# Kernel tuning notes

Measured on AMD Instinct MI355X. Metric: run time of the kernel, lower is better.

The kernel has to match this reference:

```python
import jax, jax.numpy as jnp
import numpy as np

N = 50000        # nodes
E = 800000       # edges (before self-loops)
A_DIM = 128      # attribute dim (= a_hid)
S_DIM = 64       # structural dim (= s_hid)
L = 4            # num_layers


def setup_inputs() -> dict:
    key = jax.random.key(0)
    ks = jax.random.split(key, 10)
    sc = 0.05
    return {
        "x": jax.random.normal(ks[0], (N, A_DIM), jnp.float32),
        "s": jax.random.normal(ks[1], (N, S_DIM), jnp.float32),
        "edge_index": jax.random.randint(ks[2], (2, E), 0, N, dtype=jnp.int64),
        "gcn_W": jax.random.normal(ks[3], (L, A_DIM, A_DIM), jnp.float32) * sc,
        "gcn_b": jnp.zeros((L, A_DIM), jnp.float32),
        "gna_w1W": jax.random.normal(ks[4], (L, S_DIM, S_DIM), jnp.float32) * sc,
        "gna_w1b": jnp.zeros((L, S_DIM), jnp.float32),
        "gna_w2W": jax.random.normal(ks[5], (L, S_DIM, S_DIM), jnp.float32) * sc,
        "gna_w2b": jnp.zeros((L, S_DIM), jnp.float32),
        "gna_a": jax.random.normal(ks[6], (L, S_DIM), jnp.float32) * sc,
    }


def _gelu(v):
    return jax.nn.gelu(v, approximate=False)  # matches torch F.gelu default


def _self_loops(edge_index, n):
    loop = jnp.arange(n, dtype=edge_index.dtype)
    row = jnp.concatenate([edge_index[0], loop])  # src
    col = jnp.concatenate([edge_index[1], loop])  # dst
    return row, col


def _guide_forward(x, s, edge_index, gcn_W, gcn_b,
                   gna_w1W, gna_w1b, gna_w2W, gna_w2b, gna_a):
    n = x.shape[0]
    row, col = _self_loops(edge_index, n)  # [E+N]

    # ---- attribute autoencoder: GCN with symmetric normalization ----
    deg = jax.ops.segment_sum(jnp.ones_like(col, dtype=x.dtype), col, num_segments=n)
    dinv = jnp.where(deg > 0, jax.lax.rsqrt(deg), 0.0)
    norm = dinv[row] * dinv[col]                       # [E+N]
    h = x
    for i in range(L):
        h2 = h @ gcn_W[i]                              # [N, A]
        agg = jax.ops.segment_sum(norm[:, None] * h2[row], col, num_segments=n)
        h = agg + gcn_b[i]
        if i < L - 1:                                  # jk=None: no act after last
            h = _gelu(h)

    # ---- structure autoencoder: GNA with edge-softmax attention ----
    g = s
    for i in range(L):
        t = g @ gna_w2W[i] + gna_w2b[i]                # w2(s), [N, S]
        # alpha_e = (t_dst - t_src) @ a, softmax over edges grouped by dst
        alpha = (t[col] - t[row]) @ gna_a[i]           # [E+N]
        amax = jax.ops.segment_max(alpha, col, num_segments=n)
        e = jnp.exp(alpha - amax[col])
        denom = jax.ops.segment_sum(e, col, num_segments=n)
        w = e / (denom[col] + 1e-16)
        msg = jax.ops.segment_sum(w[:, None] * t[row], col, num_segments=n)
        out = g @ gna_w1W[i] + gna_w1b[i] + msg
        g = _gelu(out)                                 # act applied after every layer
    return h, g


def reference(x, s, edge_index, gcn_W, gcn_b,
              gna_w1W, gna_w1b, gna_w2W, gna_w2b, gna_a):
    return _guide_forward(x, s, edge_index, gcn_W, gcn_b,
                          gna_w1W, gna_w1b, gna_w2W, gna_w2b, gna_a)
```

## Files before the change

### kernel.cpp

```cpp
#include <hip/hip_runtime.h>
#include <hip/hip_fp16.h>
#include <math.h>

#define N_NODES 50000
#define E_EDGES 800000
#define ET (E_EDGES + N_NODES)
#define L_LAYERS 4
#define NB_SCAN ((N_NODES + 255) / 256)
#define MF2_BLOCKS ((N_NODES + 127) / 128)
#define AGG_BLOCKS ((N_NODES / 2 * 64 + 255) / 256)

typedef __attribute__((ext_vector_type(8))) short short8;
typedef __attribute__((ext_vector_type(4))) float f32x4;

__device__ __forceinline__ float gelu_f(float x) {
    float z = fabsf(x) * 0.70710678118654752f;
    float t = __fdividef(1.0f, fmaf(0.3275911f, z, 1.0f));
    float p = t * fmaf(t, fmaf(t, fmaf(t, fmaf(t, 1.061405429f, -1.453152027f),
                                       1.421413741f), -0.284496736f),
                       0.254829592f);
    float e = __expf(-z * z);
    float erfz = copysignf(fmaf(-p, e, 1.0f), x);
    return 0.5f * x * (1.0f + erfz);
}

__device__ __forceinline__ void split_hl(float x, unsigned short& h, unsigned short& lo) {
    unsigned u = __float_as_uint(x);
    h = (unsigned short)(u >> 16);
    float hif = __uint_as_float(u & 0xffff0000u);
    lo = (unsigned short)(__float_as_uint(x - hif) >> 16);
}

__device__ __forceinline__ void fma8h(const float4& raw, float m, float* acc) {
    const __half2* h = reinterpret_cast<const __half2*>(&raw);
#pragma unroll
    for (int i = 0; i < 4; ++i) {
        float2 f = __half22float2(h[i]);
        acc[2 * i]     = fmaf(f.x, m, acc[2 * i]);
        acc[2 * i + 1] = fmaf(f.y, m, acc[2 * i + 1]);
    }
}


__global__ __launch_bounds__(256) void count_pos(const int* __restrict__ ecol,
                                                 int* __restrict__ cnt,
                                                 int* __restrict__ aux) {
    int e = blockIdx.x * 256 + threadIdx.x;
    if (e >= ET) return;
    int c = (e < E_EDGES) ? ecol[e] : (e - E_EDGES);
    aux[e] = atomicAdd(&cnt[c], 1);
}

__global__ __launch_bounds__(256) void scan_part1(const int* __restrict__ cnt,
                                                  int* __restrict__ bsum) {
    __shared__ int red[256];
    int t = threadIdx.x;
    int i = blockIdx.x * 256 + t;
    red[t] = (i < N_NODES) ? cnt[i] : 0;
    __syncthreads();
#pragma unroll
    for (int off = 128; off; off >>= 1) {
        if (t < off) red[t] += red[t + off];
        __syncthreads();
    }
    if (t == 0) bsum[blockIdx.x] = red[0];
}

__global__ __launch_bounds__(256) void scan_part3(const int* __restrict__ cnt,
                                                  const int* __restrict__ bsum,
                                                  int* __restrict__ ptrb,
                                                  float* __restrict__ dinv) {
    __shared__ int red[256];
    __shared__ int sh[256];
    int t = threadIdx.x;
    red[t] = (t < (int)blockIdx.x) ? bsum[t] : 0;
    __syncthreads();
#pragma unroll
    for (int off = 128; off; off >>= 1) {
        if (t < off) red[t] += red[t + off];
        __syncthreads();
    }
    int base = red[0];
    int i = blockIdx.x * 256 + t;
    int v = (i < N_NODES) ? cnt[i] : 0;
    sh[t] = v;
    __syncthreads();
    for (int off = 1; off < 256; off <<= 1) {
        int u = (t >= off) ? sh[t - off] : 0;
        __syncthreads();
        sh[t] += u;
        __syncthreads();
    }
    int excl = sh[t] - v + base;
    if (i < N_NODES) {
        ptrb[i] = excl;
        dinv[i] = rsqrtf((float)v);
    }
    if (i == N_NODES - 1) ptrb[N_NODES] = excl + v;
}

__global__ __launch_bounds__(256) void bucket(const int* __restrict__ erow,
                                              const int* __restrict__ ecol,
                                              const int* __restrict__ aux,
                                              const int* __restrict__ ptrb,
                                              int* __restrict__ eidx) {
    int e = blockIdx.x * 256 + threadIdx.x;
    if (e >= ET) return;
    int r, c;
    if (e < E_EDGES) { r = erow[e]; c = ecol[e]; }
    else             { r = e - E_EDGES; c = r; }
    int pos = ptrb[c] + aux[e];
    eidx[pos] = r;
}


__global__ __launch_bounds__(256) void prep_w(const float* __restrict__ gcn_W,
                                              const float* __restrict__ w1W,
                                              const float* __restrict__ w2W,
                                              unsigned short* __restrict__ gf_hi,
                                              unsigned short* __restrict__ gf_lo,
                                              unsigned short* __restrict__ nf_hi,
                                              unsigned short* __restrict__ nf_lo) {
    int idx = blockIdx.x * 256 + threadIdx.x;
    if (idx < 8192) {
        int lane = idx & 63, nt = (idx >> 6) & 7, s = (idx >> 9) & 3, layer = idx >> 11;
        int q = lane >> 4, n = lane & 15;
        const float* W = gcn_W + (size_t)layer * 128 * 128;
        size_t o = (size_t)idx * 8;
#pragma unroll
        for (int j = 0; j < 8; ++j) {
            float x = W[(size_t)(s * 32 + q * 8 + j) * 128 + nt * 16 + n];
            unsigned short h, lo;
            split_hl(x, h, lo);
            gf_hi[o + j] = h; gf_lo[o + j] = lo;
        }
    } else if (idx < 8192 + 4096) {
        int t = idx - 8192;
        int lane = t & 63, nt = (t >> 6) & 7, s = (t >> 9) & 1, layer = t >> 10;
        int q = lane >> 4, n = lane & 15;
        int col = nt * 16 + n;
        const float* W = (col < 64) ? (w1W + (size_t)layer * 64 * 64)
                                    : (w2W + (size_t)layer * 64 * 64);
        int c = col & 63;
        size_t o = (size_t)t * 8;
#pragma unroll
        for (int j = 0; j < 8; ++j) {
            float x = W[(size_t)(s * 32 + q * 8 + j) * 64 + c];
            unsigned short h, lo;
            split_hl(x, h, lo);
            nf_hi[o + j] = h; nf_lo[o + j] = lo;
        }
    }
}


__device__ __forceinline__ void mfma_steps2(const float* __restrict__ A, int Kfull,
                                            int nsteps,
                                            const unsigned short* __restrict__ wfh,
                                            const unsigned short* __restrict__ wfl,
                                            const int* arow, const bool* avalid,
                                            int lq, int l, f32x4 acc[2][8]) {
    for (int s = 0; s < nsteps; ++s) {
        short8 ah[2], al[2];
#pragma unroll
        for (int g = 0; g < 2; ++g) {
            float4 a0 = make_float4(0.f, 0.f, 0.f, 0.f);
            float4 a1 = make_float4(0.f, 0.f, 0.f, 0.f);
            if (avalid[g]) {
                const float* ap = A + (size_t)arow[g] * Kfull + s * 32 + lq * 8;
                a0 = *(const float4*)ap;
                a1 = *(const float4*)(ap + 4);
            }
            float xs[8] = {a0.x, a0.y, a0.z, a0.w, a1.x, a1.y, a1.z, a1.w};
#pragma unroll
            for (int c = 0; c < 8; ++c) {
                unsigned short h, lo;
                split_hl(xs[c], h, lo);
                ah[g][c] = (short)h; al[g][c] = (short)lo;
            }
        }
#pragma unroll
        for (int nt = 0; nt < 8; ++nt) {
            size_t fo = ((size_t)(s * 8 + nt) * 64 + l) * 8;
            short8 wh = *(const short8*)(wfh + fo);
            short8 wl = *(const short8*)(wfl + fo);
#pragma unroll
            for (int g = 0; g < 2; ++g) {
                acc[g][nt] = __builtin_amdgcn_mfma_f32_16x16x32_bf16(ah[g], wh, acc[g][nt], 0, 0, 0);
                acc[g][nt] = __builtin_amdgcn_mfma_f32_16x16x32_bf16(ah[g], wl, acc[g][nt], 0, 0, 0);
                acc[g][nt] = __builtin_amdgcn_mfma_f32_16x16x32_bf16(al[g], wh, acc[g][nt], 0, 0, 0);
            }
        }
    }
}


__global__ __launch_bounds__(256) void gemm_both(
    const float* __restrict__ A0, const float* __restrict__ A1,
    const unsigned short* __restrict__ gfh, const unsigned short* __restrict__ gfl,
    const unsigned short* __restrict__ nfh, const unsigned short* __restrict__ nfl,
    const float* __restrict__ b1, const float* __restrict__ b2,
    const float* __restrict__ avec, const float* __restrict__ dinv,
    __half* __restrict__ h2, float* __restrict__ baseb,
    __half* __restrict__ ut, float* __restrict__ ub) {
    int tid = threadIdx.x;
    int w  = tid >> 6;
    int l  = tid & 63;
    int lq = l >> 4;
    int ln = l & 15;
    bool isg = blockIdx.x >= MF2_BLOCKS;
    int blk = isg ? (blockIdx.x - MF2_BLOCKS) : blockIdx.x;
    int m0 = blk * 128;
    int arow[2];
    bool avalid[2];
#pragma unroll
    for (int g = 0; g < 2; ++g) {
        arow[g] = m0 + w * 32 + g * 16 + ln;
        avalid[g] = arow[g] < N_NODES;
    }

    f32x4 acc[2][8];
#pragma unroll
    for (int g = 0; g < 2; ++g)
#pragma unroll
        for (int i = 0; i < 8; ++i) acc[g][i] = (f32x4){0.f, 0.f, 0.f, 0.f};

    if (!isg) {
        mfma_steps2(A0, 128, 4, gfh, gfl, arow, avalid, lq, l, acc);
#pragma unroll
        for (int g = 0; g < 2; ++g) {
            float dv[4];
#pragma unroll
            for (int r = 0; r < 4; ++r) {
                int row = m0 + w * 32 + g * 16 + lq * 4 + r;
                dv[r] = (row < N_NODES) ? dinv[row] : 0.f;
            }
#pragma unroll
            for (int nt = 0; nt < 8; ++nt) {
                int col = nt * 16 + ln;
#pragma unroll
                for (int r = 0; r < 4; ++r) {
                    int row = m0 + w * 32 + g * 16 + lq * 4 + r;
                    if (row < N_NODES)
                        h2[(size_t)row * 128 + col] = __float2half(acc[g][nt][r] * dv[r]);
                }
            }
        }
    } else {
        mfma_steps2(A1, 64, 2, nfh, nfl, arow, avalid, lq, l, acc);
#pragma unroll
        for (int g = 0; g < 2; ++g) {
#pragma unroll
            for (int nt = 0; nt < 4; ++nt) {
                int col = nt * 16 + ln;
                float bb = b1[col];
#pragma unroll
                for (int r = 0; r < 4; ++r) {
                    int row = m0 + w * 32 + g * 16 + lq * 4 + r;
                    if (row < N_NODES) baseb[(size_t)row * 64 + col] = acc[g][nt][r] + bb;
                }
            }
            float pa[4] = {0.f, 0.f, 0.f, 0.f};
            float t2s[4][4];
#pragma unroll
            for (int nt = 4; nt < 8; ++nt) {
                int col = (nt - 4) * 16 + ln;
                float bb = b2[col];
                float av = avec[col];
#pragma unroll
                for (int r = 0; r < 4; ++r) {
                    float t2 = acc[g][nt][r] + bb;
                    t2s[nt - 4][r] = t2;
                    pa[r] += t2 * av;
                }
            }
#pragma unroll
            for (int r = 0; r < 4; ++r) {
                pa[r] += __shfl_xor(pa[r], 1);
                pa[r] += __shfl_xor(pa[r], 2);
                pa[r] += __shfl_xor(pa[r], 4);
                pa[r] += __shfl_xor(pa[r], 8);
            }
            float ur[4];
#pragma unroll
            for (int r = 0; r < 4; ++r) ur[r] = expf(-pa[r]);
#pragma unroll
            for (int nt = 0; nt < 4; ++nt) {
                int col = nt * 16 + ln;
#pragma unroll
                for (int r = 0; r < 4; ++r) {
                    int row = m0 + w * 32 + g * 16 + lq * 4 + r;
                    if (row < N_NODES)
                        ut[(size_t)row * 64 + col] = __float2half(t2s[nt][r] * ur[r]);
                }
            }
            if (ln == 0) {
#pragma unroll
                for (int r = 0; r < 4; ++r) {
                    int row = m0 + w * 32 + g * 16 + lq * 4 + r;
                    if (row < N_NODES) ub[row] = ur[r];
                }
            }
        }
    }
}


__global__ __launch_bounds__(256) void agg_gcn(const __half* __restrict__ h2,
                                               const int* __restrict__ ptrb,
                                               const int* __restrict__ eidx,
                                               const float* __restrict__ dinv,
                                               const float* __restrict__ bias,
                                               float* __restrict__ out,
                                               int apply_gelu) {
    int widx = (blockIdx.x * 256 + (int)threadIdx.x) >> 6;
    int lane = threadIdx.x & 63;
    int half = lane >> 5;
    int hl   = lane & 31;
    int dst  = widx * 2 + half;
    if (dst >= N_NODES) return;
    int sub = hl >> 4;
    int fl  = hl & 15;
    int p0 = ptrb[dst], p1 = ptrb[dst + 1];
    float acc[8];
#pragma unroll
    for (int i = 0; i < 8; ++i) acc[i] = 0.f;
    for (int p = p0; p < p1; p += 32) {
        int nb = min(32, p1 - p);
        int srcs = (hl < nb) ? eidx[p + hl] : 0;
        for (int eb = 0; eb < nb; eb += 16) {
            int   sv[8];
            float mk[8];
#pragma unroll
            for (int k = 0; k < 8; ++k) {
                int e = eb + sub + 2 * k;
                int c = half * 32 + min(e, nb - 1);
                sv[k] = __shfl(srcs, c);
                mk[k] = (e < nb) ? 1.f : 0.f;
            }
            float4 raw[8];
#pragma unroll
            for (int k = 0; k < 8; ++k)
                raw[k] = *(const float4*)(h2 + (size_t)sv[k] * 128 + fl * 8);
#pragma unroll
            for (int k = 0; k < 8; ++k) fma8h(raw[k], mk[k], acc);
        }
    }
#pragma unroll
    for (int i = 0; i < 8; ++i) acc[i] += __shfl_xor(acc[i], 16);
    {
        float dd = dinv[dst];
        int c0 = fl * 8 + 4 * sub;
        float4 bb = *(const float4*)(bias + c0);
        float v0 = fmaf(dd, acc[4 * sub + 0], bb.x);
        float v1 = fmaf(dd, acc[4 * sub + 1], bb.y);
        float v2 = fmaf(dd, acc[4 * sub + 2], bb.z);
        float v3 = fmaf(dd, acc[4 * sub + 3], bb.w);
        if (apply_gelu) {
            v0 = gelu_f(v0); v1 = gelu_f(v1); v2 = gelu_f(v2); v3 = gelu_f(v3);
        }
        *(float4*)(out + (size_t)dst * 128 + c0) = make_float4(v0, v1, v2, v3);
    }
}


__global__ __launch_bounds__(256) void gna_agg(const __half* __restrict__ ut,
                                               const float* __restrict__ ub,
                                               const int* __restrict__ ptrb,
                                               const int* __restrict__ eidx,
                                               const float* __restrict__ base,
                                               float* __restrict__ gout) {
    int widx = (blockIdx.x * 256 + (int)threadIdx.x) >> 6;
    int lane = threadIdx.x & 63;
    int half = lane >> 5;
    int hl   = lane & 31;
    int dst  = widx * 2 + half;
    if (dst >= N_NODES) return;
    int sub = hl >> 3;
    int fl  = hl & 7;
    int p0 = ptrb[dst], p1 = ptrb[dst + 1];
    float se = 0.f;
    float acc[8];
#pragma unroll
    for (int i = 0; i < 8; ++i) acc[i] = 0.f;
    for (int p = p0; p < p1; p += 32) {
        int nb = min(32, p1 - p);
        int srcs = (hl < nb) ? eidx[p + hl] : 0;
        if (hl < nb) se += ub[srcs];
        int   sv[8];
        float mk[8];
#pragma unroll
        for (int k = 0; k < 8; ++k) {
            int e = sub + 4 * k;
            int c = half * 32 + min(e, nb - 1);
            sv[k] = __shfl(srcs, c);
            mk[k] = (e < nb) ? 1.f : 0.f;
        }
        float4 raw[8];
#pragma unroll
        for (int k = 0; k < 8; ++k)
            raw[k] = *(const float4*)(ut + (size_t)sv[k] * 64 + fl * 8);
#pragma unroll
        for (int k = 0; k < 8; ++k) fma8h(raw[k], mk[k], acc);
    }
#pragma unroll
    for (int off = 1; off <= 16; off <<= 1) se += __shfl_xor(se, off);
#pragma unroll
    for (int off = 8; off <= 16; off <<= 1)
#pragma unroll
        for (int i = 0; i < 8; ++i) acc[i] += __shfl_xor(acc[i], off);
    {
        float winv = __fdividef(1.0f, se + 1e-16f);
        int c0 = fl * 8 + 2 * sub;
        float2 bs = *(const float2*)(base + (size_t)dst * 64 + c0);
        float v0 = gelu_f(fmaf(acc[2 * sub + 0], winv, bs.x));
        float v1 = gelu_f(fmaf(acc[2 * sub + 1], winv, bs.y));
        *(float2*)(gout + (size_t)dst * 64 + c0) = make_float2(v0, v1);
    }
}


extern "C" void kernel_launch(void* const* d_in, const int* in_sizes, int n_in,
                              void* d_out, int out_size, void* d_ws, size_t ws_size,
                              hipStream_t stream) {
    const float* x     = (const float*)d_in[0];
    const float* s     = (const float*)d_in[1];
    const int*   ei    = (const int*)d_in[2];
    const float* gcn_W = (const float*)d_in[3];
    const float* gcn_b = (const float*)d_in[4];
    const float* w1W   = (const float*)d_in[5];
    const float* w1b   = (const float*)d_in[6];
    const float* w2W   = (const float*)d_in[7];
    const float* w2b   = (const float*)d_in[8];
    const float* ga    = (const float*)d_in[9];

    float* h_out = (float*)d_out;
    float* g_out = (float*)d_out + (size_t)N_NODES * 128;

    size_t off = 0;
    char* wsb = (char*)d_ws;
    auto take = [&](size_t bytes) {
        void* p = wsb + off;
        off = (off + bytes + 255) & ~(size_t)255;
        return p;
    };
    int*    cnt     = (int*)take((size_t)N_NODES * 4);
    int*    ptrb    = (int*)take((size_t)(N_NODES + 1) * 4);
    int*    aux     = (int*)take((size_t)ET * 4);
    float*  dinv    = (float*)take((size_t)N_NODES * 4);
    int*    eidx    = (int*)take((size_t)ET * 4);
    __half* h2      = (__half*)take((size_t)N_NODES * 128 * 2);
    __half* utbuf   = (__half*)take((size_t)N_NODES * 64 * 2);
    float*  basebuf = (float*)take((size_t)N_NODES * 64 * 4);
    float*  ubuf    = (float*)take((size_t)N_NODES * 4);
    int*    bsum    = (int*)take((size_t)NB_SCAN * 4);
    unsigned short* gf_hi = (unsigned short*)take((size_t)8192 * 8 * 2);
    unsigned short* gf_lo = (unsigned short*)take((size_t)8192 * 8 * 2);
    unsigned short* nf_hi = (unsigned short*)take((size_t)4096 * 8 * 2);
    unsigned short* nf_lo = (unsigned short*)take((size_t)4096 * 8 * 2);
    (void)ws_size; (void)in_sizes; (void)n_in; (void)out_size;

    const int* erow = ei;
    const int* ecol = ei + E_EDGES;

    hipMemsetAsync(cnt, 0, (size_t)N_NODES * 4, stream);

    int ge = (ET + 255) / 256;
    count_pos<<<ge, 256, 0, stream>>>(ecol, cnt, aux);
    scan_part1<<<NB_SCAN, 256, 0, stream>>>(cnt, bsum);
    scan_part3<<<NB_SCAN, 256, 0, stream>>>(cnt, bsum, ptrb, dinv);
    bucket<<<ge, 256, 0, stream>>>(erow, ecol, aux, ptrb, eidx);
    prep_w<<<48, 256, 0, stream>>>(gcn_W, w1W, w2W, gf_hi, gf_lo, nf_hi, nf_lo);

    const float* hin = x;
    const float* gin = s;
    for (int l = 0; l < L_LAYERS; ++l) {
        gemm_both<<<2 * MF2_BLOCKS, 256, 0, stream>>>(
            hin, gin,
            gf_hi + (size_t)l * 4 * 8 * 64 * 8, gf_lo + (size_t)l * 4 * 8 * 64 * 8,
            nf_hi + (size_t)l * 2 * 8 * 64 * 8, nf_lo + (size_t)l * 2 * 8 * 64 * 8,
            w1b + (size_t)l * 64, w2b + (size_t)l * 64, ga + (size_t)l * 64, dinv,
            h2, basebuf, utbuf, ubuf);
        agg_gcn<<<AGG_BLOCKS, 256, 0, stream>>>(
            h2, ptrb, eidx, dinv, gcn_b + (size_t)l * 128, h_out,
            (l < L_LAYERS - 1) ? 1 : 0);
        gna_agg<<<AGG_BLOCKS, 256, 0, stream>>>(
            utbuf, ubuf, ptrb, eidx, basebuf, g_out);
        hin = h_out;
        gin = g_out;
    }
}
```

Before: 480.1 us.

## Stage GEMM input and output tiles through LDS with 64-row blocks

The fused GEMM kernel now uses 64-row tiles instead of 128, which doubles the block count and halves the per-wave accumulator state. Input rows are loaded cooperatively into padded shared memory, and MFMA operands are read from there rather than gathered per lane from global memory. Results are written back through shared memory so global stores are full 16-byte row segments instead of scattered 2- or 4-byte stores. The cost is extra barriers and LDS traffic, and the weight fragments are now reread for every 64 rows rather than every 128.

```diff
diff --git a/kernel.cpp b/kernel.cpp
--- a/kernel.cpp
+++ b/kernel.cpp
@@ -7,7 +7,7 @@
 #define ET (E_EDGES + N_NODES)
 #define L_LAYERS 4
 #define NB_SCAN ((N_NODES + 255) / 256)
-#define MF2_BLOCKS ((N_NODES + 127) / 128)
+#define MF_BLOCKS ((N_NODES + 63) / 64)
 #define AGG_BLOCKS ((N_NODES / 2 * 64 + 255) / 256)
 
 typedef __attribute__((ext_vector_type(8))) short short8;
@@ -154,42 +154,32 @@
 }
 
 
-__device__ __forceinline__ void mfma_steps2(const float* __restrict__ A, int Kfull,
-                                            int nsteps,
-                                            const unsigned short* __restrict__ wfh,
-                                            const unsigned short* __restrict__ wfl,
-                                            const int* arow, const bool* avalid,
-                                            int lq, int l, f32x4 acc[2][8]) {
+__device__ __forceinline__ void mfma_steps_lds(const float* __restrict__ lda, int ldp,
+                                               int nsteps,
+                                               const unsigned short* __restrict__ wfh,
+                                               const unsigned short* __restrict__ wfl,
+                                               int lrow, int lq, int l,
+                                               f32x4* acc) {
     for (int s = 0; s < nsteps; ++s) {
-        short8 ah[2], al[2];
-#pragma unroll
-        for (int g = 0; g < 2; ++g) {
-            float4 a0 = make_float4(0.f, 0.f, 0.f, 0.f);
-            float4 a1 = make_float4(0.f, 0.f, 0.f, 0.f);
-            if (avalid[g]) {
-                const float* ap = A + (size_t)arow[g] * Kfull + s * 32 + lq * 8;
-                a0 = *(const float4*)ap;
-                a1 = *(const float4*)(ap + 4);
-            }
-            float xs[8] = {a0.x, a0.y, a0.z, a0.w, a1.x, a1.y, a1.z, a1.w};
-#pragma unroll
-            for (int c = 0; c < 8; ++c) {
-                unsigned short h, lo;
-                split_hl(xs[c], h, lo);
-                ah[g][c] = (short)h; al[g][c] = (short)lo;
-            }
+        const float* ap = lda + lrow * ldp + s * 32 + lq * 8;
+        float4 a0 = *(const float4*)ap;
+        float4 a1 = *(const float4*)(ap + 4);
+        float xs[8] = {a0.x, a0.y, a0.z, a0.w, a1.x, a1.y, a1.z, a1.w};
+        short8 ah, al;
+#pragma unroll
+        for (int c = 0; c < 8; ++c) {
+            unsigned short h, lo;
+            split_hl(xs[c], h, lo);
+            ah[c] = (short)h; al[c] = (short)lo;
         }
 #pragma unroll
         for (int nt = 0; nt < 8; ++nt) {
             size_t fo = ((size_t)(s * 8 + nt) * 64 + l) * 8;
             short8 wh = *(const short8*)(wfh + fo);
             short8 wl = *(const short8*)(wfl + fo);
-#pragma unroll
-            for (int g = 0; g < 2; ++g) {
-                acc[g][nt] = __builtin_amdgcn_mfma_f32_16x16x32_bf16(ah[g], wh, acc[g][nt], 0, 0, 0);
-                acc[g][nt] = __builtin_amdgcn_mfma_f32_16x16x32_bf16(ah[g], wl, acc[g][nt], 0, 0, 0);
-                acc[g][nt] = __builtin_amdgcn_mfma_f32_16x16x32_bf16(al[g], wh, acc[g][nt], 0, 0, 0);
-            }
+            acc[nt] = __builtin_amdgcn_mfma_f32_16x16x32_bf16(ah, wh, acc[nt], 0, 0, 0);
+            acc[nt] = __builtin_amdgcn_mfma_f32_16x16x32_bf16(ah, wl, acc[nt], 0, 0, 0);
+            acc[nt] = __builtin_amdgcn_mfma_f32_16x16x32_bf16(al, wh, acc[nt], 0, 0, 0);
         }
     }
 }
@@ -203,36 +193,50 @@
     const float* __restrict__ avec, const float* __restrict__ dinv,
     __half* __restrict__ h2, float* __restrict__ baseb,
     __half* __restrict__ ut, float* __restrict__ ub) {
+    __shared__ __align__(16) char smem[33792];
     int tid = threadIdx.x;
     int w  = tid >> 6;
     int l  = tid & 63;
     int lq = l >> 4;
     int ln = l & 15;
-    bool isg = blockIdx.x >= MF2_BLOCKS;
-    int blk = isg ? (blockIdx.x - MF2_BLOCKS) : blockIdx.x;
-    int m0 = blk * 128;
-    int arow[2];
-    bool avalid[2];
-#pragma unroll
-    for (int g = 0; g < 2; ++g) {
-        arow[g] = m0 + w * 32 + g * 16 + ln;
-        avalid[g] = arow[g] < N_NODES;
-    }
-
-    f32x4 acc[2][8];
-#pragma unroll
-    for (int g = 0; g < 2; ++g)
-#pragma unroll
-        for (int i = 0; i < 8; ++i) acc[g][i] = (f32x4){0.f, 0.f, 0.f, 0.f};
+    bool isg = blockIdx.x >= MF_BLOCKS;
+    int blk = isg ? (blockIdx.x - MF_BLOCKS) : blockIdx.x;
+    int m0 = blk * 64;
+    const float* A = isg ? A1 : A0;
+    const int Kfull = isg ? 64 : 128;
+    const int ldp   = isg ? 68 : 132;
+    float* lda = (float*)smem;
+
+    {
+        int row = tid >> 2, q = tid & 3;
+        int grow = m0 + row;
+        int hw = Kfull >> 2;
+        float4* dst = (float4*)(lda + row * ldp + q * hw);
+        int nv = hw >> 2;
+        if (grow < N_NODES) {
+            const float4* src = (const float4*)(A + (size_t)grow * Kfull + q * hw);
+            for (int i = 0; i < nv; ++i) dst[i] = src[i];
+        } else {
+            for (int i = 0; i < nv; ++i) dst[i] = make_float4(0.f, 0.f, 0.f, 0.f);
+        }
+    }
+    __syncthreads();
+
+    f32x4 acc[8];
+#pragma unroll
+    for (int i = 0; i < 8; ++i) acc[i] = (f32x4){0.f, 0.f, 0.f, 0.f};
+
+    int lrow = w * 16 + ln;
 
     if (!isg) {
-        mfma_steps2(A0, 128, 4, gfh, gfl, arow, avalid, lq, l, acc);
-#pragma unroll
-        for (int g = 0; g < 2; ++g) {
+        mfma_steps_lds(lda, 132, 4, gfh, gfl, lrow, lq, l, acc);
+        __syncthreads();
+        __half* ldc = (__half*)smem;
+        {
             float dv[4];
 #pragma unroll
             for (int r = 0; r < 4; ++r) {
-                int row = m0 + w * 32 + g * 16 + lq * 4 + r;
+                int row = m0 + w * 16 + lq * 4 + r;
                 dv[r] = (row < N_NODES) ? dinv[row] : 0.f;
             }
 #pragma unroll
@@ -240,24 +244,36 @@
                 int col = nt * 16 + ln;
 #pragma unroll
                 for (int r = 0; r < 4; ++r) {
-                    int row = m0 + w * 32 + g * 16 + lq * 4 + r;
-                    if (row < N_NODES)
-                        h2[(size_t)row * 128 + col] = __float2half(acc[g][nt][r] * dv[r]);
+                    int lr = w * 16 + lq * 4 + r;
+                    ldc[lr * 128 + col] = __float2half(acc[nt][r] * dv[r]);
                 }
             }
         }
+        __syncthreads();
+        {
+            int row = tid >> 2, seg = tid & 3;
+            int grow = m0 + row;
+            if (grow < N_NODES) {
+                const uint4* src = (const uint4*)(ldc + row * 128 + seg * 32);
+                uint4* dst = (uint4*)(h2 + (size_t)grow * 128 + seg * 32);
+#pragma unroll
+                for (int i = 0; i < 4; ++i) dst[i] = src[i];
+            }
+        }
     } else {
-        mfma_steps2(A1, 64, 2, nfh, nfl, arow, avalid, lq, l, acc);
-#pragma unroll
-        for (int g = 0; g < 2; ++g) {
+        mfma_steps_lds(lda, 68, 2, nfh, nfl, lrow, lq, l, acc);
+        __syncthreads();
+        float* ldf = (float*)smem;
+        __half* ldh = (__half*)(smem + 16384);
+        {
 #pragma unroll
             for (int nt = 0; nt < 4; ++nt) {
                 int col = nt * 16 + ln;
                 float bb = b1[col];
 #pragma unroll
                 for (int r = 0; r < 4; ++r) {
-                    int row = m0 + w * 32 + g * 16 + lq * 4 + r;
-                    if (row < N_NODES) baseb[(size_t)row * 64 + col] = acc[g][nt][r] + bb;
+                    int lr = w * 16 + lq * 4 + r;
+                    ldf[lr * 64 + col] = acc[nt][r] + bb;
                 }
             }
             float pa[4] = {0.f, 0.f, 0.f, 0.f};
@@ -269,7 +285,7 @@
                 float av = avec[col];
 #pragma unroll
                 for (int r = 0; r < 4; ++r) {
-                    float t2 = acc[g][nt][r] + bb;
+                    float t2 = acc[nt][r] + bb;
                     t2s[nt - 4][r] = t2;
                     pa[r] += t2 * av;
                 }
@@ -289,17 +305,31 @@
                 int col = nt * 16 + ln;
 #pragma unroll
                 for (int r = 0; r < 4; ++r) {
-                    int row = m0 + w * 32 + g * 16 + lq * 4 + r;
-                    if (row < N_NODES)
-                        ut[(size_t)row * 64 + col] = __float2half(t2s[nt][r] * ur[r]);
+                    int lr = w * 16 + lq * 4 + r;
+                    ldh[lr * 64 + col] = __float2half(t2s[nt][r] * ur[r]);
                 }
             }
             if (ln == 0) {
 #pragma unroll
                 for (int r = 0; r < 4; ++r) {
-                    int row = m0 + w * 32 + g * 16 + lq * 4 + r;
+                    int row = m0 + w * 16 + lq * 4 + r;
                     if (row < N_NODES) ub[row] = ur[r];
                 }
+            }
+        }
+        __syncthreads();
+        {
+            int row = tid >> 2, seg = tid & 3;
+            int grow = m0 + row;
+            if (grow < N_NODES) {
+                const uint4* src = (const uint4*)(ldf + row * 64 + seg * 16);
+                uint4* dst = (uint4*)(baseb + (size_t)grow * 64 + seg * 16);
+#pragma unroll
+                for (int i = 0; i < 4; ++i) dst[i] = src[i];
+                const uint4* srh = (const uint4*)(ldh + row * 64 + seg * 16);
+                uint4* dsh = (uint4*)(ut + (size_t)grow * 64 + seg * 16);
+#pragma unroll
+                for (int i = 0; i < 2; ++i) dsh[i] = srh[i];
             }
         }
     }
@@ -475,7 +505,7 @@
     const float* hin = x;
     const float* gin = s;
     for (int l = 0; l < L_LAYERS; ++l) {
-        gemm_both<<<2 * MF2_BLOCKS, 256, 0, stream>>>(
+        gemm_both<<<2 * MF_BLOCKS, 256, 0, stream>>>(
             hin, gin,
             gf_hi + (size_t)l * 4 * 8 * 64 * 8, gf_lo + (size_t)l * 4 * 8 * 64 * 8,
             nf_hi + (size_t)l * 2 * 8 * 64 * 8, nf_lo + (size_t)l * 2 * 8 * 64 * 8,
```

New measurement: 469.9 us. -2.1%, faster.
